# Performance work log

Measured on AMD Instinct MI355X. Metric: run time of the kernel, lower is better.

Reference implementation:

```python
import jax, jax.numpy as jnp
import numpy as np

T_IN, A_IN, V_IN = 300, 81, 371          # fixed feature splits of x_p
T_H, A_H, V_H = 128, 64, 64              # LSTM hidden sizes
MEM = 256                                 # memory dim
ATTN_IN = 2 * (T_H + A_H + V_H)           # 512
GIN = ATTN_IN + MEM                       # 768
NN1 = NN2 = G1D = G2D = OH = 128
SEQ, BATCH = 20, 4096


def setup_inputs() -> dict:
    keys = iter(jax.random.split(jax.random.key(0), 64))
    def w(*shape):
        return jax.random.normal(next(keys), shape, dtype=jnp.float32) * 0.05
    inp = {
        "x_p": jax.random.normal(next(keys), (SEQ, BATCH, T_IN + A_IN + V_IN), dtype=jnp.float32),
        "c_t": jnp.zeros((BATCH, T_H), jnp.float32),
        "c_a": jnp.zeros((BATCH, A_H), jnp.float32),
        "c_v": jnp.zeros((BATCH, V_H), jnp.float32),
        "mem": jnp.zeros((BATCH, MEM), jnp.float32),
        "t_Wih": w(4 * T_H, T_IN), "t_Whh": w(4 * T_H, T_H), "t_b": w(4 * T_H),
        "a_Wih": w(4 * A_H, A_IN), "a_Whh": w(4 * A_H, A_H), "a_b": w(4 * A_H),
        "v_Wih": w(4 * V_H, V_IN), "v_Whh": w(4 * V_H, V_H), "v_b": w(4 * V_H),
        "attn1_W1": w(NN1, ATTN_IN), "attn1_b1": w(NN1), "attn1_W2": w(ATTN_IN, NN1), "attn1_b2": w(ATTN_IN),
        "attn2_W1": w(NN2, ATTN_IN), "attn2_b1": w(NN2), "attn2_W2": w(MEM, NN2), "attn2_b2": w(MEM),
        "g1_W1": w(G1D, GIN), "g1_b1": w(G1D), "g1_W2": w(MEM, G1D), "g1_b2": w(MEM),
        "g2_W1": w(G2D, GIN), "g2_b1": w(G2D), "g2_W2": w(MEM, G2D), "g2_b2": w(MEM),
        "out_W1": w(OH, T_H + A_H + V_H + MEM), "out_b1": w(OH), "out_W2": w(1, OH), "out_b2": w(1),
    }
    return inp


def _lstm(x, h, c, Wih, Whh, b):
    # torch.nn.LSTMCell: gates ordered i, f, g, o; b = b_ih + b_hh
    z = x @ Wih.T + h @ Whh.T + b
    i, f, g, o = jnp.split(z, 4, axis=1)
    c2 = jax.nn.sigmoid(f) * c + jax.nn.sigmoid(i) * jnp.tanh(g)
    return jax.nn.sigmoid(o) * jnp.tanh(c2), c2


def _mlp(x, W1, b1, W2, b2):
    # fc2(relu(fc1(x))); dropout is identity in eval mode
    return jax.nn.relu(x @ W1.T + b1) @ W2.T + b2


def reference(x_p, c_t, c_a, c_v, mem,
              t_Wih, t_Whh, t_b, a_Wih, a_Whh, a_b, v_Wih, v_Whh, v_b,
              attn1_W1, attn1_b1, attn1_W2, attn1_b2,
              attn2_W1, attn2_b1, attn2_W2, attn2_b2,
              g1_W1, g1_b1, g1_W2, g1_b2,
              g2_W1, g2_b1, g2_W2, g2_b2,
              out_W1, out_b1, out_W2, out_b2):
    n = x_p.shape[1]
    init = (jnp.zeros((n, T_H), x_p.dtype), c_t,
            jnp.zeros((n, A_H), x_p.dtype), c_a,
            jnp.zeros((n, V_H), x_p.dtype), c_v, mem)

    def step(carry, x_t):
        t_h, t_c, a_h, a_c, v_h, v_c, m = carry
        pre_c = jnp.concatenate([t_c, a_c, v_c], axis=1)
        nt_h, nt_c = _lstm(x_t[:, :T_IN], t_h, t_c, t_Wih, t_Whh, t_b)
        na_h, na_c = _lstm(x_t[:, T_IN:T_IN + A_IN], a_h, a_c, a_Wih, a_Whh, a_b)
        nv_h, nv_c = _lstm(x_t[:, T_IN + A_IN:], v_h, v_c, v_Wih, v_Whh, v_b)
        cur_c = jnp.concatenate([nt_c, na_c, nv_c], axis=1)
        c_star = jnp.concatenate([pre_c, cur_c], axis=1)            # [n, 512]
        attn = jax.nn.softmax(_mlp(c_star, attn1_W1, attn1_b1, attn1_W2, attn1_b2), axis=1)
        attended = attn * c_star
        c_hat = jnp.tanh(_mlp(attended, attn2_W1, attn2_b1, attn2_W2, attn2_b2))
        both = jnp.concatenate([attended, m], axis=1)               # [n, 768]
        gamma1 = jax.nn.sigmoid(_mlp(both, g1_W1, g1_b1, g1_W2, g1_b2))
        gamma2 = jax.nn.sigmoid(_mlp(both, g2_W1, g2_b1, g2_W2, g2_b2))
        m = gamma1 * m + gamma2 * c_hat
        return (nt_h, nt_c, na_h, na_c, nv_h, nv_c, m), None

    (t_h, _, a_h, _, v_h, _, m), _ = jax.lax.scan(step, init, x_p)
    last_h = jnp.concatenate([t_h, a_h, v_h, m], axis=1)            # [n, 512]
    return _mlp(last_h, out_W1, out_b1, out_W2, out_b2)             # [n, 1]
```

## Files before the change

kernel.cpp:

```cpp
#include <hip/hip_runtime.h>
#include <math.h>

typedef _Float16 f16;
typedef f16 f16x4 __attribute__((ext_vector_type(4)));
typedef f16 f16x8 __attribute__((ext_vector_type(8)));
typedef float f32x4 __attribute__((ext_vector_type(4)));

#define MFMA16(a, b, c) __builtin_amdgcn_mfma_f32_16x16x32_f16((a), (b), (c), 0, 0, 0)


struct PackArgs {
  const float *t_Wih, *t_Whh, *t_b, *a_Wih, *a_Whh, *a_b, *v_Wih, *v_Whh, *v_b;
  const float *aW1, *aW2, *bW1, *bW2, *g1W1, *g2W1, *g1W2, *g2W2, *oW1;
  f16 *Wx_t, *Wx_a, *Wx_v, *Wh_t, *Wh_a, *Wh_v;
  f16 *W_a1, *W_a2, *W_b1, *W_b2, *W_g1, *W_g2, *W_o1;
  float *bg;
};

__device__ __forceinline__ void fdec(int e, int NK, int& row, int& col) {
  int t = e / (NK * 512);
  int r = e % (NK * 512);
  int ks = r >> 9;
  int lane = (r & 511) >> 3;
  int j = r & 7;
  row = t * 16 + (lane & 15);
  col = 32 * ks + 8 * (lane >> 4) + j;
}

__global__ __launch_bounds__(256) void pack_w(PackArgs p) {
  int idx = blockIdx.x * 256 + threadIdx.x;
  int row, col;
  if (idx < 163840) {
    fdec(idx, 10, row, col);
    int srow = (row & 3) * 128 + (row >> 2);
    p.Wx_t[idx] = (f16)((col < 300) ? p.t_Wih[srow * 300 + col] : 0.f);
    return;
  }
  idx -= 163840;
  if (idx < 24576) {
    fdec(idx, 3, row, col);
    int srow = (row & 3) * 64 + (row >> 2);
    p.Wx_a[idx] = (f16)((col < 81) ? p.a_Wih[srow * 81 + col] : 0.f);
    return;
  }
  idx -= 24576;
  if (idx < 98304) {
    fdec(idx, 12, row, col);
    int srow = (row & 3) * 64 + (row >> 2);
    p.Wx_v[idx] = (f16)((col < 371) ? p.v_Wih[srow * 371 + col] : 0.f);
    return;
  }
  idx -= 98304;
  if (idx < 65536) {
    fdec(idx, 4, row, col);
    int srow = (row & 3) * 128 + (row >> 2);
    p.Wh_t[idx] = (f16)p.t_Whh[srow * 128 + col];
    return;
  }
  idx -= 65536;
  if (idx < 16384) {
    fdec(idx, 2, row, col);
    int srow = (row & 3) * 64 + (row >> 2);
    p.Wh_a[idx] = (f16)p.a_Whh[srow * 64 + col];
    return;
  }
  idx -= 16384;
  if (idx < 16384) {
    fdec(idx, 2, row, col);
    int srow = (row & 3) * 64 + (row >> 2);
    p.Wh_v[idx] = (f16)p.v_Whh[srow * 64 + col];
    return;
  }
  idx -= 16384;
  if (idx < 65536) { fdec(idx, 16, row, col); p.W_a1[idx] = (f16)p.aW1[row * 512 + col]; return; }
  idx -= 65536;
  if (idx < 65536) { fdec(idx, 4, row, col); p.W_a2[idx] = (f16)p.aW2[row * 128 + col]; return; }
  idx -= 65536;
  if (idx < 65536) { fdec(idx, 16, row, col); p.W_b1[idx] = (f16)p.bW1[row * 512 + col]; return; }
  idx -= 65536;
  if (idx < 32768) { fdec(idx, 4, row, col); p.W_b2[idx] = (f16)p.bW2[row * 128 + col]; return; }
  idx -= 32768;
  if (idx < 196608) {
    fdec(idx, 24, row, col);
    p.W_g1[idx] = (f16)((row < 128) ? p.g1W1[row * 768 + col] : p.g2W1[(row - 128) * 768 + col]);
    return;
  }
  idx -= 196608;
  if (idx < 65536) {
    fdec(idx, 4, row, col);
    p.W_g2[idx] = (f16)((row < 256) ? p.g1W2[row * 128 + col] : p.g2W2[(row - 256) * 128 + col]);
    return;
  }
  idx -= 65536;
  if (idx < 65536) { fdec(idx, 16, row, col); p.W_o1[idx] = (f16)p.oW1[row * 512 + col]; return; }
  idx -= 65536;
  if (idx < 1024) {
    int n = idx;
    float v;
    if (n < 512)      v = p.t_b[(n & 3) * 128 + (n >> 2)];
    else if (n < 768) { int m = n - 512; v = p.a_b[(m & 3) * 64 + (m >> 2)]; }
    else              { int m = n - 768; v = p.v_b[(m & 3) * 64 + (m >> 2)]; }
    p.bg[n] = v;
  }
}

struct ZxArgs { const float* x; const f16 *Wx_t, *Wx_a, *Wx_v; f16* zx; int t0; };

template <int KS, int XOFF>
__device__ __forceinline__ void zx_wave(const f16* __restrict__ Wx, int nt0, int n0g,
                                        const f16 (*Xs)[808], f16* __restrict__ zx,
                                        int mloc, int lane, int l15, int lg) {
#pragma unroll 1
  for (int half = 0; half < 2; ++half) {
    f32x4 acc[8];
#pragma unroll
    for (int j = 0; j < 8; ++j) acc[j] = (f32x4){0.f, 0.f, 0.f, 0.f};
#pragma unroll 1
    for (int ks = 0; ks < KS; ++ks) {
      f16x8 w[4];
#pragma unroll
      for (int i = 0; i < 4; ++i)
        w[i] = *(const f16x8*)(Wx + (size_t)((nt0 + 4 * half + i) * KS + ks) * 512 + lane * 8);
      f16x8 a0 = *(const f16x8*)(&Xs[l15][XOFF + 32 * ks + 8 * lg]);
      f16x8 a1 = *(const f16x8*)(&Xs[16 + l15][XOFF + 32 * ks + 8 * lg]);
#pragma unroll
      for (int i = 0; i < 4; ++i) {
        acc[i] = MFMA16(a0, w[i], acc[i]);
        acc[4 + i] = MFMA16(a1, w[i], acc[4 + i]);
      }
    }
#pragma unroll
    for (int mt = 0; mt < 2; ++mt)
#pragma unroll
      for (int i = 0; i < 4; ++i) {
        int ng = n0g + 64 * half + 16 * i + l15;
#pragma unroll
        for (int q = 0; q < 4; ++q)
          zx[(size_t)(mloc + mt * 16 + 4 * lg + q) * 1024 + ng] = (f16)acc[mt * 4 + i][q];
      }
  }
}

__global__ __launch_bounds__(512, 2) void gemm_zx(ZxArgs z) {
  __shared__ f16 Xs[32][808];
  const int tid = threadIdx.x, wid = tid >> 6, lane = tid & 63, l15 = lane & 15, lg = lane >> 4;
  const int mloc = blockIdx.x * 32;
  {
    int r = tid >> 4;
    const float* xr = z.x + ((size_t)z.t0 * 4096 + mloc + r) * 752;
    for (int c = tid & 15; c < 800; c += 16) {
      float v;
      if (c < 320)      v = (c < 300) ? xr[c] : 0.f;
      else if (c < 416) { int s = c - 320; v = (s < 81) ? xr[300 + s] : 0.f; }
      else              { int s = c - 416; v = (s < 371) ? xr[381 + s] : 0.f; }
      Xs[r][c] = (f16)v;
    }
  }
  __syncthreads();
  if (wid < 4)
    zx_wave<10, 0>(z.Wx_t, 8 * wid, 128 * wid, Xs, z.zx, mloc, lane, l15, lg);
  else if (wid < 6)
    zx_wave<3, 320>(z.Wx_a, 8 * (wid - 4), 512 + 128 * (wid - 4), Xs, z.zx, mloc, lane, l15, lg);
  else
    zx_wave<12, 416>(z.Wx_v, 8 * (wid - 6), 768 + 128 * (wid - 6), Xs, z.zx, mloc, lane, l15, lg);
}

struct MainArgs {
  const float *x_p, *c_t, *c_a, *c_v, *mem0;
  const f16 *Wh_t, *Wh_a, *Wh_v, *W_a1, *W_a2, *W_b1, *W_b2, *W_g1, *W_g2, *W_o1;
  const float *bg, *a1b1, *a1b2, *a2b1, *a2b2, *g1b1, *g1b2, *g2b1, *g2b2, *ob1, *oW2, *ob2;
  f16 *Hst; float *Cst, *Mst; const f16 *zx;
  float *out;
};

__device__ __forceinline__ float sigm(float x) {
  return __builtin_amdgcn_rcpf(1.f + __expf(-x));
}
__device__ __forceinline__ float ftanh(float x) {
  float t = __expf(-2.f * fabsf(x));
  float r = (1.f - t) * __builtin_amdgcn_rcpf(1.f + t);
  return copysignf(r, x);
}

template <int KS, int LDA>
__device__ __forceinline__ f32x4 fc_tileF(const f16 (*Asrc)[LDA], int acol,
                                          const f16* Wtile, int lane, int l15, int lg) {
  f32x4 acc = {0.f, 0.f, 0.f, 0.f};
  constexpr int GB = (KS < 8) ? KS : 8;
  constexpr int G = (KS + GB - 1) / GB;
#pragma unroll
  for (int g = 0; g < G; ++g) {
    f16x8 w[GB];
#pragma unroll
    for (int j = 0; j < GB; ++j)
      w[j] = *(const f16x8*)(Wtile + (size_t)(g * GB + j) * 512 + lane * 8);
#pragma unroll
    for (int j = 0; j < GB; ++j) {
      f16x8 a = *(const f16x8*)(&Asrc[l15][acol + 8 * lg + 32 * (g * GB + j)]);
      acc = MFMA16(a, w[j], acc);
    }
  }
  return acc;
}

template <int KSH>
__device__ __forceinline__ void gmm_zxB(const f16* Wh, const float* bg, const f16* zxr,
                                        int nc0, int n0, int cub,
                                        int l15, int lg, int hb, int lane,
                                        const f16 (*hc)[264], f16 (*hn)[264],
                                        float (*cS)[260], f16 (*bufA)[808]) {
  f16x8 ah[KSH];
#pragma unroll
  for (int k = 0; k < KSH; ++k)
    ah[k] = *(const f16x8*)(&hc[l15][hb + 8 * lg + 32 * k]);
#pragma unroll 1
  for (int p = 0; p < 4; ++p) {
    const int tau = (nc0 >> 4) + 2 * p;
    f16x8 w0[KSH], w1[KSH];
#pragma unroll
    for (int k = 0; k < KSH; ++k) {
      w0[k] = *(const f16x8*)(Wh + (size_t)(tau * KSH + k) * 512 + lane * 8);
      w1[k] = *(const f16x8*)(Wh + (size_t)((tau + 1) * KSH + k) * 512 + lane * 8);
    }
    f16x4 z0 = *(const f16x4*)(zxr + n0 + 32 * p + 4 * lg);
    f16x4 z1 = *(const f16x4*)(zxr + n0 + 32 * p + 16 + 4 * lg);
    f32x4 a0 = {0.f, 0.f, 0.f, 0.f}, a1 = {0.f, 0.f, 0.f, 0.f};
#pragma unroll
    for (int k = 0; k < KSH; ++k) {
      a0 = MFMA16(w0[k], ah[k], a0);
      a1 = MFMA16(w1[k], ah[k], a1);
    }
    const float4 b0 = *(const float4*)&bg[n0 + 32 * p + 4 * lg];
    const float4 b1 = *(const float4*)&bg[n0 + 32 * p + 16 + 4 * lg];
    {
      float gi = sigm(a0[0] + (float)z0[0] + b0.x);
      float gf = sigm(a0[1] + (float)z0[1] + b0.y);
      float gg = ftanh(a0[2] + (float)z0[2] + b0.z);
      float go = sigm(a0[3] + (float)z0[3] + b0.w);
      int cu = cub + ((nc0 + 32 * p) >> 2) + lg;
      float cold = cS[l15][cu];
      float cnew = gf * cold + gi * gg;
      cS[l15][cu] = cnew;
      hn[l15][cu] = (f16)(go * ftanh(cnew));
      bufA[l15][cu] = (f16)cold;
      bufA[l15][256 + cu] = (f16)cnew;
    }
    {
      float gi = sigm(a1[0] + (float)z1[0] + b1.x);
      float gf = sigm(a1[1] + (float)z1[1] + b1.y);
      float gg = ftanh(a1[2] + (float)z1[2] + b1.z);
      float go = sigm(a1[3] + (float)z1[3] + b1.w);
      int cu = cub + ((nc0 + 32 * p + 16) >> 2) + lg;
      float cold = cS[l15][cu];
      float cnew = gf * cold + gi * gg;
      cS[l15][cu] = cnew;
      hn[l15][cu] = (f16)(go * ftanh(cnew));
      bufA[l15][cu] = (f16)cold;
      bufA[l15][256 + cu] = (f16)cnew;
    }
  }
}

__global__ __launch_bounds__(512, 2) void fused_seq(MainArgs A, int cs,
                                                    int first, int last) {
  __shared__ f16  h16a[16][264];
  __shared__ f16  h16b[16][264];
  __shared__ float cS[16][260];
  __shared__ float mS[16][260];
  __shared__ f16  bufA[16][808];
  __shared__ f16  hid16[16][264];
  __shared__ f16  ghid16[16][264];
  __shared__ float zf[16][516];

  const int tid = threadIdx.x;
  const int wid = tid >> 6, lane = tid & 63, l15 = lane & 15, lg = lane >> 4;
  const int r0 = blockIdx.x * 16;

  f16 (*hc)[264] = h16a;
  f16 (*hn)[264] = h16b;

  if (first) {
    for (int idx = tid; idx < 4096; idx += 512) {
      int r = idx >> 8, c = idx & 255, R = r0 + r;
      h16a[r][c] = (f16)0.f;
      float cv = (c < 128) ? A.c_t[R * 128 + c]
                           : (c < 192 ? A.c_a[R * 64 + c - 128] : A.c_v[R * 64 + c - 192]);
      cS[r][c] = cv;
      mS[r][c] = A.mem0[R * 256 + c];
    }
  } else {
    for (int idx = tid; idx < 4096; idx += 512) {
      int r = idx >> 8, c = idx & 255;
      size_t g = (size_t)(r0 + r) * 256 + c;
      h16a[r][c] = A.Hst[g];
      cS[r][c] = A.Cst[g];
      mS[r][c] = A.Mst[g];
    }
  }
  __syncthreads();

#pragma unroll 1
  for (int ts = 0; ts < cs; ++ts) {
    {
      const f16* zxr = A.zx + ((size_t)ts * 4096 + r0 + l15) * 1024;
      if (wid < 4)
        gmm_zxB<4>(A.Wh_t, A.bg, zxr, 128 * wid, 128 * wid, 0,
                   l15, lg, 0, lane, hc, hn, cS, bufA);
      else if (wid < 6)
        gmm_zxB<2>(A.Wh_a, A.bg, zxr, 128 * (wid - 4), 512 + 128 * (wid - 4), 128,
                   l15, lg, 128, lane, hc, hn, cS, bufA);
      else
        gmm_zxB<2>(A.Wh_v, A.bg, zxr, 128 * (wid - 6), 768 + 128 * (wid - 6), 192,
                   l15, lg, 192, lane, hc, hn, cS, bufA);
    }
    __syncthreads();

    {
      int n = 16 * wid;
      f32x4 acc = fc_tileF<16, 808>(bufA, 0, A.W_a1 + (size_t)wid * 16 * 512, lane, l15, lg);
      float b = A.a1b1[n + l15];
#pragma unroll
      for (int q = 0; q < 4; ++q) hid16[lg * 4 + q][n + l15] = (f16)fmaxf(acc[q] + b, 0.f);
    }
    __syncthreads();

    {
#pragma unroll
      for (int i = 0; i < 4; ++i) {
        int tt = 4 * wid + i;
        int n = 16 * tt + l15;
        f32x4 acc = fc_tileF<4, 264>(hid16, 0, A.W_a2 + (size_t)tt * 4 * 512, lane, l15, lg);
        float b = A.a1b2[n];
#pragma unroll
        for (int q = 0; q < 4; ++q) zf[lg * 4 + q][n] = acc[q] + b;
      }
    }
    __syncthreads();

    {
      int row = tid >> 5, c0 = tid & 31;
      float v[16]; float mx = -1e30f;
#pragma unroll
      for (int j = 0; j < 16; ++j) { v[j] = zf[row][c0 + 32 * j]; mx = fmaxf(mx, v[j]); }
#pragma unroll
      for (int m = 1; m < 32; m <<= 1) mx = fmaxf(mx, __shfl_xor(mx, m));
      float s = 0.f;
#pragma unroll
      for (int j = 0; j < 16; ++j) { v[j] = __expf(v[j] - mx); s += v[j]; }
#pragma unroll
      for (int m = 1; m < 32; m <<= 1) s += __shfl_xor(s, m);
      float inv = __builtin_amdgcn_rcpf(s);
#pragma unroll
      for (int j = 0; j < 16; ++j) {
        int c = c0 + 32 * j;
        bufA[row][c] = (f16)(v[j] * inv * (float)bufA[row][c]);
      }
      for (int idx = tid; idx < 4096; idx += 512) {
        int r = idx >> 8, c = idx & 255;
        bufA[r][512 + c] = (f16)mS[r][c];
      }
    }
    __syncthreads();

    {
#pragma unroll 1
      for (int i = 0; i < 2; ++i) {
        int tt = 2 * wid + i;
        int nn = 16 * tt + l15;
        f32x4 acc = fc_tileF<24, 808>(bufA, 0, A.W_g1 + (size_t)tt * 24 * 512, lane, l15, lg);
        float b = (nn < 128) ? A.g1b1[nn] : A.g2b1[nn - 128];
#pragma unroll
        for (int q = 0; q < 4; ++q) ghid16[lg * 4 + q][nn] = (f16)fmaxf(acc[q] + b, 0.f);
      }
      {
        int n = 16 * wid;
        f32x4 acc = fc_tileF<16, 808>(bufA, 0, A.W_b1 + (size_t)wid * 16 * 512, lane, l15, lg);
        float b = A.a2b1[n + l15];
#pragma unroll
        for (int q = 0; q < 4; ++q) hid16[lg * 4 + q][n + l15] = (f16)fmaxf(acc[q] + b, 0.f);
      }
    }
    __syncthreads();

    {
#pragma unroll 1
      for (int i = 0; i < 2; ++i) {
        int tt = 2 * wid + i;
        int n = 16 * tt + l15;
        f16x8 wB[4], w1[4], w2[4];
#pragma unroll
        for (int k = 0; k < 4; ++k) {
          wB[k] = *(const f16x8*)(A.W_b2 + (size_t)(tt * 4 + k) * 512 + lane * 8);
          w1[k] = *(const f16x8*)(A.W_g2 + (size_t)(tt * 4 + k) * 512 + lane * 8);
          w2[k] = *(const f16x8*)(A.W_g2 + (size_t)((16 + tt) * 4 + k) * 512 + lane * 8);
        }
        f32x4 acB = {0.f, 0.f, 0.f, 0.f};
        f32x4 ac1 = {0.f, 0.f, 0.f, 0.f};
        f32x4 ac2 = {0.f, 0.f, 0.f, 0.f};
#pragma unroll
        for (int k = 0; k < 4; ++k) {
          f16x8 ha = *(const f16x8*)(&hid16[l15][8 * lg + 32 * k]);
          f16x8 ga1 = *(const f16x8*)(&ghid16[l15][8 * lg + 32 * k]);
          f16x8 ga2 = *(const f16x8*)(&ghid16[l15][128 + 8 * lg + 32 * k]);
          acB = MFMA16(ha, wB[k], acB);
          ac1 = MFMA16(ga1, w1[k], ac1);
          ac2 = MFMA16(ga2, w2[k], ac2);
        }
        float bB = A.a2b2[n], b1 = A.g1b2[n], b2 = A.g2b2[n];
#pragma unroll
        for (int q = 0; q < 4; ++q) {
          int row = lg * 4 + q;
          float ch = ftanh(acB[q] + bB);
          float g1 = sigm(ac1[q] + b1);
          float g2 = sigm(ac2[q] + b2);
          mS[row][n] = g1 * mS[row][n] + g2 * ch;
        }
      }
    }
    __syncthreads();

    { f16 (*tmp)[264] = hc; hc = hn; hn = tmp; }
  }

  if (last) {
    for (int idx = tid; idx < 4096; idx += 512) {
      int r = idx >> 8, c = idx & 255;
      bufA[r][c] = hc[r][c];
      bufA[r][256 + c] = (f16)mS[r][c];
    }
    __syncthreads();
    {
      int n = 16 * wid;
      f32x4 acc = fc_tileF<16, 808>(bufA, 0, A.W_o1 + (size_t)wid * 16 * 512, lane, l15, lg);
      float b = A.ob1[n + l15];
#pragma unroll
      for (int q = 0; q < 4; ++q) hid16[lg * 4 + q][n + l15] = (f16)fmaxf(acc[q] + b, 0.f);
    }
    __syncthreads();
    {
      int row = tid >> 5, c0 = tid & 31;
      float s = 0.f;
#pragma unroll
      for (int j = 0; j < 4; ++j) { int k = c0 + 32 * j; s += (float)hid16[row][k] * A.oW2[k]; }
#pragma unroll
      for (int m = 1; m < 32; m <<= 1) s += __shfl_xor(s, m);
      if (c0 == 0) A.out[r0 + row] = s + A.ob2[0];
    }
  } else {
    for (int idx = tid; idx < 4096; idx += 512) {
      int r = idx >> 8, c = idx & 255;
      size_t g = (size_t)(r0 + r) * 256 + c;
      A.Hst[g] = hc[r][c];
      A.Cst[g] = cS[r][c];
      A.Mst[g] = mS[r][c];
    }
  }
}

extern "C" void kernel_launch(void* const* d_in, const int* in_sizes, int n_in,
                              void* d_out, int out_size, void* d_ws, size_t ws_size,
                              hipStream_t stream) {
  (void)in_sizes; (void)n_in; (void)out_size;
  char* w = (char*)d_ws;
  f16* Wx_t = (f16*)(w + 0);
  f16* Wx_a = (f16*)(w + 327680);
  f16* Wx_v = (f16*)(w + 376832);
  f16* Wh_t = (f16*)(w + 573440);
  f16* Wh_a = (f16*)(w + 704512);
  f16* Wh_v = (f16*)(w + 737280);
  f16* W_a1 = (f16*)(w + 770048);
  f16* W_a2 = (f16*)(w + 901120);
  f16* W_b1 = (f16*)(w + 1032192);
  f16* W_b2 = (f16*)(w + 1163264);
  f16* W_g1 = (f16*)(w + 1228800);
  f16* W_g2 = (f16*)(w + 1622016);
  f16* W_o1 = (f16*)(w + 1753088);
  float* bg = (float*)(w + 1884160);
  f16* Hst = (f16*)(w + 1888256);
  float* Cst = (float*)(w + 3985408);
  float* Mst = (float*)(w + 8179712);
  f16* zx = (f16*)(w + 12374016);

  size_t avail = (ws_size > 12374016) ? ws_size - 12374016 : 0;
  const size_t per_step = (size_t)4096 * 1024 * 2;
  int cs = 1;
  const int divs[6] = {20, 10, 5, 4, 2, 1};
  for (int i = 0; i < 6; ++i)
    if ((size_t)divs[i] * per_step <= avail) { cs = divs[i]; break; }

  PackArgs pa;
  pa.t_Wih = (const float*)d_in[5];  pa.t_Whh = (const float*)d_in[6];  pa.t_b = (const float*)d_in[7];
  pa.a_Wih = (const float*)d_in[8];  pa.a_Whh = (const float*)d_in[9];  pa.a_b = (const float*)d_in[10];
  pa.v_Wih = (const float*)d_in[11]; pa.v_Whh = (const float*)d_in[12]; pa.v_b = (const float*)d_in[13];
  pa.aW1 = (const float*)d_in[14];  pa.aW2 = (const float*)d_in[16];
  pa.bW1 = (const float*)d_in[18];  pa.bW2 = (const float*)d_in[20];
  pa.g1W1 = (const float*)d_in[22]; pa.g2W1 = (const float*)d_in[26];
  pa.g1W2 = (const float*)d_in[24]; pa.g2W2 = (const float*)d_in[28];
  pa.oW1 = (const float*)d_in[30];
  pa.Wx_t = Wx_t; pa.Wx_a = Wx_a; pa.Wx_v = Wx_v;
  pa.Wh_t = Wh_t; pa.Wh_a = Wh_a; pa.Wh_v = Wh_v;
  pa.W_a1 = W_a1; pa.W_a2 = W_a2; pa.W_b1 = W_b1; pa.W_b2 = W_b2;
  pa.W_g1 = W_g1; pa.W_g2 = W_g2; pa.W_o1 = W_o1;
  pa.bg = bg;
  pack_w<<<3684, 256, 0, stream>>>(pa);

  MainArgs ma;
  ma.x_p = (const float*)d_in[0];
  ma.c_t = (const float*)d_in[1]; ma.c_a = (const float*)d_in[2]; ma.c_v = (const float*)d_in[3];
  ma.mem0 = (const float*)d_in[4];
  ma.Wh_t = Wh_t; ma.Wh_a = Wh_a; ma.Wh_v = Wh_v;
  ma.W_a1 = W_a1; ma.W_a2 = W_a2; ma.W_b1 = W_b1; ma.W_b2 = W_b2;
  ma.W_g1 = W_g1; ma.W_g2 = W_g2; ma.W_o1 = W_o1;
  ma.bg = bg;
  ma.a1b1 = (const float*)d_in[15]; ma.a1b2 = (const float*)d_in[17];
  ma.a2b1 = (const float*)d_in[19]; ma.a2b2 = (const float*)d_in[21];
  ma.g1b1 = (const float*)d_in[23]; ma.g1b2 = (const float*)d_in[25];
  ma.g2b1 = (const float*)d_in[27]; ma.g2b2 = (const float*)d_in[29];
  ma.ob1 = (const float*)d_in[31]; ma.oW2 = (const float*)d_in[32]; ma.ob2 = (const float*)d_in[33];
  ma.Hst = Hst; ma.Cst = Cst; ma.Mst = Mst; ma.zx = zx;
  ma.out = (float*)d_out;

  for (int t0 = 0; t0 < 20; t0 += cs) {
    ZxArgs za; za.x = (const float*)d_in[0];
    za.Wx_t = Wx_t; za.Wx_a = Wx_a; za.Wx_v = Wx_v; za.zx = zx; za.t0 = t0;
    gemm_zx<<<dim3(cs * 128), 512, 0, stream>>>(za);
    fused_seq<<<256, 512, 0, stream>>>(ma, cs, t0 == 0 ? 1 : 0,
                                       (t0 + cs >= 20) ? 1 : 0);
  }
}
```

Baseline: 541.8 us.

## Double fused_seq block to 1024 threads, splitting per-step GEMMs across 16 waves

Raises the recurrent kernel's block size from 512 to 1024 threads, so 16 waves instead of 8 each take a share of every per-timestep stage. The LSTM recurrence covers half as many gate pairs per wave, and the attention first layers are split along K with partial sums reduced through shared memory. Softmax and the output reduction now use one full wave per row. The goal is to shorten the serial per-step latency with more parallel work, at the cost of extra barriers, an added reduction pass, and launch bounds that allow only one block per CU with a tighter register budget.

```diff
diff --git a/kernel.cpp b/kernel.cpp
--- a/kernel.cpp
+++ b/kernel.cpp
@@ -182,8 +182,8 @@
   return copysignf(r, x);
 }
 
-template <int KS, int LDA>
-__device__ __forceinline__ f32x4 fc_tileF(const f16 (*Asrc)[LDA], int acol,
+template <int KS, int KOFF, int LDA>
+__device__ __forceinline__ f32x4 fc_tileF(const f16 (*Asrc)[LDA],
                                           const f16* Wtile, int lane, int l15, int lg) {
   f32x4 acc = {0.f, 0.f, 0.f, 0.f};
   constexpr int GB = (KS < 8) ? KS : 8;
@@ -193,17 +193,17 @@
     f16x8 w[GB];
 #pragma unroll
     for (int j = 0; j < GB; ++j)
-      w[j] = *(const f16x8*)(Wtile + (size_t)(g * GB + j) * 512 + lane * 8);
+      w[j] = *(const f16x8*)(Wtile + (size_t)(KOFF + g * GB + j) * 512 + lane * 8);
 #pragma unroll
     for (int j = 0; j < GB; ++j) {
-      f16x8 a = *(const f16x8*)(&Asrc[l15][acol + 8 * lg + 32 * (g * GB + j)]);
+      f16x8 a = *(const f16x8*)(&Asrc[l15][8 * lg + 32 * (KOFF + g * GB + j)]);
       acc = MFMA16(a, w[j], acc);
     }
   }
   return acc;
 }
 
-template <int KSH>
+template <int KSH, int PAIRS>
 __device__ __forceinline__ void gmm_zxB(const f16* Wh, const float* bg, const f16* zxr,
                                         int nc0, int n0, int cub,
                                         int l15, int lg, int hb, int lane,
@@ -214,7 +214,7 @@
   for (int k = 0; k < KSH; ++k)
     ah[k] = *(const f16x8*)(&hc[l15][hb + 8 * lg + 32 * k]);
 #pragma unroll 1
-  for (int p = 0; p < 4; ++p) {
+  for (int p = 0; p < PAIRS; ++p) {
     const int tau = (nc0 >> 4) + 2 * p;
     f16x8 w0[KSH], w1[KSH];
 #pragma unroll
@@ -261,8 +261,8 @@
   }
 }
 
-__global__ __launch_bounds__(512, 2) void fused_seq(MainArgs A, int cs,
-                                                    int first, int last) {
+__global__ __launch_bounds__(1024, 1) void fused_seq(MainArgs A, int cs,
+                                                     int first, int last) {
   __shared__ f16  h16a[16][264];
   __shared__ f16  h16b[16][264];
   __shared__ float cS[16][260];
@@ -279,8 +279,11 @@
   f16 (*hc)[264] = h16a;
   f16 (*hn)[264] = h16b;
 
+  const int a1t = wid & 7;
+  const int kh = wid >> 3;
+
   if (first) {
-    for (int idx = tid; idx < 4096; idx += 512) {
+    for (int idx = tid; idx < 4096; idx += 1024) {
       int r = idx >> 8, c = idx & 255, R = r0 + r;
       h16a[r][c] = (f16)0.f;
       float cv = (c < 128) ? A.c_t[R * 128 + c]
@@ -289,7 +292,7 @@
       mS[r][c] = A.mem0[R * 256 + c];
     }
   } else {
-    for (int idx = tid; idx < 4096; idx += 512) {
+    for (int idx = tid; idx < 4096; idx += 1024) {
       int r = idx >> 8, c = idx & 255;
       size_t g = (size_t)(r0 + r) * 256 + c;
       h16a[r][c] = A.Hst[g];
@@ -303,118 +306,122 @@
   for (int ts = 0; ts < cs; ++ts) {
     {
       const f16* zxr = A.zx + ((size_t)ts * 4096 + r0 + l15) * 1024;
-      if (wid < 4)
-        gmm_zxB<4>(A.Wh_t, A.bg, zxr, 128 * wid, 128 * wid, 0,
-                   l15, lg, 0, lane, hc, hn, cS, bufA);
-      else if (wid < 6)
-        gmm_zxB<2>(A.Wh_a, A.bg, zxr, 128 * (wid - 4), 512 + 128 * (wid - 4), 128,
-                   l15, lg, 128, lane, hc, hn, cS, bufA);
+      if (wid < 8)
+        gmm_zxB<4, 2>(A.Wh_t, A.bg, zxr, 64 * wid, 64 * wid, 0,
+                      l15, lg, 0, lane, hc, hn, cS, bufA);
+      else if (wid < 12)
+        gmm_zxB<2, 2>(A.Wh_a, A.bg, zxr, 64 * (wid - 8), 512 + 64 * (wid - 8), 128,
+                      l15, lg, 128, lane, hc, hn, cS, bufA);
       else
-        gmm_zxB<2>(A.Wh_v, A.bg, zxr, 128 * (wid - 6), 768 + 128 * (wid - 6), 192,
-                   l15, lg, 192, lane, hc, hn, cS, bufA);
-    }
-    __syncthreads();
-
-    {
-      int n = 16 * wid;
-      f32x4 acc = fc_tileF<16, 808>(bufA, 0, A.W_a1 + (size_t)wid * 16 * 512, lane, l15, lg);
-      float b = A.a1b1[n + l15];
-#pragma unroll
-      for (int q = 0; q < 4; ++q) hid16[lg * 4 + q][n + l15] = (f16)fmaxf(acc[q] + b, 0.f);
-    }
-    __syncthreads();
-
-    {
-#pragma unroll
-      for (int i = 0; i < 4; ++i) {
-        int tt = 4 * wid + i;
-        int n = 16 * tt + l15;
-        f32x4 acc = fc_tileF<4, 264>(hid16, 0, A.W_a2 + (size_t)tt * 4 * 512, lane, l15, lg);
-        float b = A.a1b2[n];
-#pragma unroll
-        for (int q = 0; q < 4; ++q) zf[lg * 4 + q][n] = acc[q] + b;
-      }
-    }
-    __syncthreads();
-
-    {
-      int row = tid >> 5, c0 = tid & 31;
-      float v[16]; float mx = -1e30f;
-#pragma unroll
-      for (int j = 0; j < 16; ++j) { v[j] = zf[row][c0 + 32 * j]; mx = fmaxf(mx, v[j]); }
-#pragma unroll
-      for (int m = 1; m < 32; m <<= 1) mx = fmaxf(mx, __shfl_xor(mx, m));
-      float s = 0.f;
-#pragma unroll
-      for (int j = 0; j < 16; ++j) { v[j] = __expf(v[j] - mx); s += v[j]; }
-#pragma unroll
-      for (int m = 1; m < 32; m <<= 1) s += __shfl_xor(s, m);
-      float inv = __builtin_amdgcn_rcpf(s);
-#pragma unroll
-      for (int j = 0; j < 16; ++j) {
-        int c = c0 + 32 * j;
-        bufA[row][c] = (f16)(v[j] * inv * (float)bufA[row][c]);
-      }
-      for (int idx = tid; idx < 4096; idx += 512) {
-        int r = idx >> 8, c = idx & 255;
-        bufA[r][512 + c] = (f16)mS[r][c];
-      }
-    }
-    __syncthreads();
-
-    {
-#pragma unroll 1
-      for (int i = 0; i < 2; ++i) {
-        int tt = 2 * wid + i;
-        int nn = 16 * tt + l15;
-        f32x4 acc = fc_tileF<24, 808>(bufA, 0, A.W_g1 + (size_t)tt * 24 * 512, lane, l15, lg);
-        float b = (nn < 128) ? A.g1b1[nn] : A.g2b1[nn - 128];
-#pragma unroll
-        for (int q = 0; q < 4; ++q) ghid16[lg * 4 + q][nn] = (f16)fmaxf(acc[q] + b, 0.f);
-      }
-      {
-        int n = 16 * wid;
-        f32x4 acc = fc_tileF<16, 808>(bufA, 0, A.W_b1 + (size_t)wid * 16 * 512, lane, l15, lg);
-        float b = A.a2b1[n + l15];
-#pragma unroll
-        for (int q = 0; q < 4; ++q) hid16[lg * 4 + q][n + l15] = (f16)fmaxf(acc[q] + b, 0.f);
-      }
-    }
-    __syncthreads();
-
-    {
-#pragma unroll 1
+        gmm_zxB<2, 2>(A.Wh_v, A.bg, zxr, 64 * (wid - 12), 768 + 64 * (wid - 12), 192,
+                      l15, lg, 192, lane, hc, hn, cS, bufA);
+    }
+    __syncthreads();
+
+    {
+      f32x4 acc = (kh == 0)
+        ? fc_tileF<8, 0, 808>(bufA, A.W_a1 + (size_t)a1t * 16 * 512, lane, l15, lg)
+        : fc_tileF<8, 8, 808>(bufA, A.W_a1 + (size_t)a1t * 16 * 512, lane, l15, lg);
+      int n = 16 * a1t + l15;
+#pragma unroll
+      for (int q = 0; q < 4; ++q) zf[lg * 4 + q][kh * 128 + n] = acc[q];
+    }
+    __syncthreads();
+    for (int idx = tid; idx < 2048; idx += 1024) {
+      int r = idx >> 7, n = idx & 127;
+      hid16[r][n] = (f16)fmaxf(zf[r][n] + zf[r][128 + n] + A.a1b1[n], 0.f);
+    }
+    __syncthreads();
+
+    {
+#pragma unroll
       for (int i = 0; i < 2; ++i) {
         int tt = 2 * wid + i;
         int n = 16 * tt + l15;
-        f16x8 wB[4], w1[4], w2[4];
-#pragma unroll
-        for (int k = 0; k < 4; ++k) {
-          wB[k] = *(const f16x8*)(A.W_b2 + (size_t)(tt * 4 + k) * 512 + lane * 8);
-          w1[k] = *(const f16x8*)(A.W_g2 + (size_t)(tt * 4 + k) * 512 + lane * 8);
-          w2[k] = *(const f16x8*)(A.W_g2 + (size_t)((16 + tt) * 4 + k) * 512 + lane * 8);
-        }
-        f32x4 acB = {0.f, 0.f, 0.f, 0.f};
-        f32x4 ac1 = {0.f, 0.f, 0.f, 0.f};
-        f32x4 ac2 = {0.f, 0.f, 0.f, 0.f};
-#pragma unroll
-        for (int k = 0; k < 4; ++k) {
-          f16x8 ha = *(const f16x8*)(&hid16[l15][8 * lg + 32 * k]);
-          f16x8 ga1 = *(const f16x8*)(&ghid16[l15][8 * lg + 32 * k]);
-          f16x8 ga2 = *(const f16x8*)(&ghid16[l15][128 + 8 * lg + 32 * k]);
-          acB = MFMA16(ha, wB[k], acB);
-          ac1 = MFMA16(ga1, w1[k], ac1);
-          ac2 = MFMA16(ga2, w2[k], ac2);
-        }
-        float bB = A.a2b2[n], b1 = A.g1b2[n], b2 = A.g2b2[n];
-#pragma unroll
-        for (int q = 0; q < 4; ++q) {
-          int row = lg * 4 + q;
-          float ch = ftanh(acB[q] + bB);
-          float g1 = sigm(ac1[q] + b1);
-          float g2 = sigm(ac2[q] + b2);
-          mS[row][n] = g1 * mS[row][n] + g2 * ch;
-        }
+        f32x4 acc = fc_tileF<4, 0, 264>(hid16, A.W_a2 + (size_t)tt * 4 * 512, lane, l15, lg);
+        float b = A.a1b2[n];
+#pragma unroll
+        for (int q = 0; q < 4; ++q) zf[lg * 4 + q][n] = acc[q] + b;
+      }
+    }
+    __syncthreads();
+
+    {
+      int row = wid;
+      float v[8]; float mx = -1e30f;
+#pragma unroll
+      for (int j = 0; j < 8; ++j) { v[j] = zf[row][lane + 64 * j]; mx = fmaxf(mx, v[j]); }
+#pragma unroll
+      for (int m = 1; m < 64; m <<= 1) mx = fmaxf(mx, __shfl_xor(mx, m));
+      float s = 0.f;
+#pragma unroll
+      for (int j = 0; j < 8; ++j) { v[j] = __expf(v[j] - mx); s += v[j]; }
+#pragma unroll
+      for (int m = 1; m < 64; m <<= 1) s += __shfl_xor(s, m);
+      float inv = __builtin_amdgcn_rcpf(s);
+#pragma unroll
+      for (int j = 0; j < 8; ++j) {
+        int c = lane + 64 * j;
+        bufA[row][c] = (f16)(v[j] * inv * (float)bufA[row][c]);
+      }
+      for (int idx = tid; idx < 4096; idx += 1024) {
+        int r = idx >> 8, c = idx & 255;
+        bufA[r][512 + c] = (f16)mS[r][c];
+      }
+    }
+    __syncthreads();
+
+    {
+      int nn = 16 * wid + l15;
+      f32x4 acc = fc_tileF<24, 0, 808>(bufA, A.W_g1 + (size_t)wid * 24 * 512, lane, l15, lg);
+      float b = (nn < 128) ? A.g1b1[nn] : A.g2b1[nn - 128];
+#pragma unroll
+      for (int q = 0; q < 4; ++q) ghid16[lg * 4 + q][nn] = (f16)fmaxf(acc[q] + b, 0.f);
+    }
+    {
+      f32x4 acc = (kh == 0)
+        ? fc_tileF<8, 0, 808>(bufA, A.W_b1 + (size_t)a1t * 16 * 512, lane, l15, lg)
+        : fc_tileF<8, 8, 808>(bufA, A.W_b1 + (size_t)a1t * 16 * 512, lane, l15, lg);
+      int n = 16 * a1t + l15;
+#pragma unroll
+      for (int q = 0; q < 4; ++q) zf[lg * 4 + q][kh * 128 + n] = acc[q];
+    }
+    __syncthreads();
+    for (int idx = tid; idx < 2048; idx += 1024) {
+      int r = idx >> 7, n = idx & 127;
+      hid16[r][n] = (f16)fmaxf(zf[r][n] + zf[r][128 + n] + A.a2b1[n], 0.f);
+    }
+    __syncthreads();
+
+    {
+      int n = 16 * wid + l15;
+      f16x8 wB[4], w1[4], w2[4];
+#pragma unroll
+      for (int k = 0; k < 4; ++k) {
+        wB[k] = *(const f16x8*)(A.W_b2 + (size_t)(wid * 4 + k) * 512 + lane * 8);
+        w1[k] = *(const f16x8*)(A.W_g2 + (size_t)(wid * 4 + k) * 512 + lane * 8);
+        w2[k] = *(const f16x8*)(A.W_g2 + (size_t)((16 + wid) * 4 + k) * 512 + lane * 8);
+      }
+      f32x4 acB = {0.f, 0.f, 0.f, 0.f};
+      f32x4 ac1 = {0.f, 0.f, 0.f, 0.f};
+      f32x4 ac2 = {0.f, 0.f, 0.f, 0.f};
+#pragma unroll
+      for (int k = 0; k < 4; ++k) {
+        f16x8 ha = *(const f16x8*)(&hid16[l15][8 * lg + 32 * k]);
+        f16x8 ga1 = *(const f16x8*)(&ghid16[l15][8 * lg + 32 * k]);
+        f16x8 ga2 = *(const f16x8*)(&ghid16[l15][128 + 8 * lg + 32 * k]);
+        acB = MFMA16(ha, wB[k], acB);
+        ac1 = MFMA16(ga1, w1[k], ac1);
+        ac2 = MFMA16(ga2, w2[k], ac2);
+      }
+      float bB = A.a2b2[n], b1 = A.g1b2[n], b2 = A.g2b2[n];
+#pragma unroll
+      for (int q = 0; q < 4; ++q) {
+        int row = lg * 4 + q;
+        float ch = ftanh(acB[q] + bB);
+        float g1 = sigm(ac1[q] + b1);
+        float g2 = sigm(ac2[q] + b2);
+        mS[row][n] = g1 * mS[row][n] + g2 * ch;
       }
     }
     __syncthreads();
@@ -423,31 +430,30 @@
   }
 
   if (last) {
-    for (int idx = tid; idx < 4096; idx += 512) {
+    for (int idx = tid; idx < 4096; idx += 1024) {
       int r = idx >> 8, c = idx & 255;
       bufA[r][c] = hc[r][c];
       bufA[r][256 + c] = (f16)mS[r][c];
     }
     __syncthreads();
-    {
+    if (wid < 8) {
       int n = 16 * wid;
-      f32x4 acc = fc_tileF<16, 808>(bufA, 0, A.W_o1 + (size_t)wid * 16 * 512, lane, l15, lg);
+      f32x4 acc = fc_tileF<16, 0, 808>(bufA, A.W_o1 + (size_t)wid * 16 * 512, lane, l15, lg);
       float b = A.ob1[n + l15];
 #pragma unroll
       for (int q = 0; q < 4; ++q) hid16[lg * 4 + q][n + l15] = (f16)fmaxf(acc[q] + b, 0.f);
     }
     __syncthreads();
     {
-      int row = tid >> 5, c0 = tid & 31;
-      float s = 0.f;
-#pragma unroll
-      for (int j = 0; j < 4; ++j) { int k = c0 + 32 * j; s += (float)hid16[row][k] * A.oW2[k]; }
-#pragma unroll
-      for (int m = 1; m < 32; m <<= 1) s += __shfl_xor(s, m);
-      if (c0 == 0) A.out[r0 + row] = s + A.ob2[0];
+      int row = wid;
+      float s = (float)hid16[row][lane] * A.oW2[lane] +
+                (float)hid16[row][64 + lane] * A.oW2[64 + lane];
+#pragma unroll
+      for (int m = 1; m < 64; m <<= 1) s += __shfl_xor(s, m);
+      if (lane == 0) A.out[r0 + row] = s + A.ob2[0];
     }
   } else {
-    for (int idx = tid; idx < 4096; idx += 512) {
+    for (int idx = tid; idx < 4096; idx += 1024) {
       int r = idx >> 8, c = idx & 255;
       size_t g = (size_t)(r0 + r) * 256 + c;
       A.Hst[g] = hc[r][c];
@@ -524,7 +530,7 @@
     ZxArgs za; za.x = (const float*)d_in[0];
     za.Wx_t = Wx_t; za.Wx_a = Wx_a; za.Wx_v = Wx_v; za.zx = zx; za.t0 = t0;
     gemm_zx<<<dim3(cs * 128), 512, 0, stream>>>(za);
-    fused_seq<<<256, 512, 0, stream>>>(ma, cs, t0 == 0 ? 1 : 0,
-                                       (t0 + cs >= 20) ? 1 : 0);
-  }
-}
+    fused_seq<<<256, 1024, 0, stream>>>(ma, cs, t0 == 0 ? 1 : 0,
+                                        (t0 + cs >= 20) ? 1 : 0);
+  }
+}
```

Result: slower. 907.6 us (+67.5%).
